# Optimization experiments

Measured on AMD Instinct MI355X. Metric: run time of the kernel, lower is better.

Reference implementation:

```python
import jax, jax.numpy as jnp
import numpy as np

B, S, H = 2, 2048, 1024
NUM_HEAD = 16
HEAD = H // NUM_HEAD
NEG = -10000000000.0


def setup_inputs() -> dict:
    key = jax.random.key(0)
    ks = jax.random.split(key, 10)
    scale = 1.0 / np.sqrt(H)
    return {
        "query": jax.random.normal(ks[0], (B, S, H), jnp.float32),
        "key": jax.random.normal(ks[1], (B, S, H), jnp.float32),
        "value": jax.random.normal(ks[2], (B, S, H), jnp.float32),
        "mask": jax.random.randint(ks[3], (B, S), 0, 2, jnp.int32),
        "Wq": jax.random.normal(ks[4], (H, H), jnp.float32) * scale,
        "bq": jnp.zeros((H,), jnp.float32),
        "Wk": jax.random.normal(ks[5], (H, H), jnp.float32) * scale,
        "bk": jnp.zeros((H,), jnp.float32),
        "Wv": jax.random.normal(ks[6], (H, H), jnp.float32) * scale,
        "bv": jnp.zeros((H,), jnp.float32),
    }


def reference(query, key, value, mask, Wq, bq, Wk, bk, Wv, bv):
    b, s, h = query.shape
    # Linear projections (torch Linear: x @ W.T + b), split into heads -> [b, nh, s, hd]
    def proj(x, W, bias):
        y = x @ W.T + bias
        return y.reshape(b, s, NUM_HEAD, HEAD).transpose(0, 2, 1, 3)

    q = proj(query, Wq, bq)
    k = proj(key, Wk, bk)
    v = proj(value, Wv, bv)

    # NOTE: original module has NO 1/sqrt(head_dim) scaling -- faithful.
    attn_score = jnp.einsum("bhqd,bhkd->bhqk", q, k)  # [b, nh, s, s]
    # key-padding mask bias: 0 where mask==1, -1e10 where mask==0, broadcast over query dim
    bias_add = jnp.where(mask[:, None, None, :] == 0, NEG, 0.0).astype(attn_score.dtype)
    attn_score = attn_score + bias_add
    attn_ratio = jax.nn.softmax(attn_score, axis=-1)
    out = jnp.einsum("bhqk,bhkd->bhqd", attn_ratio, v)  # [b, nh, s, hd]
    out = out.transpose(0, 2, 1, 3).reshape(b, s, h)
    # Dropout is identity in eval mode; output_linear is defined but never used in forward.
    return out
```

## Files before the change

kernel.cpp:

```cpp
#include <hip/hip_runtime.h>

#define BATCH 2
#define S_LEN 2048
#define HDIM  1024
#define NHEAD 16
#define HD    64
#define NEGBIAS -1e10f

typedef __attribute__((ext_vector_type(8))) _Float16 half8;
typedef __attribute__((ext_vector_type(4))) float   f32x4;

__global__ __launch_bounds__(256) void proj_gemm_f16(
    const float* __restrict__ Xq, const float* __restrict__ Wq, const float* __restrict__ bq,
    const float* __restrict__ Xk, const float* __restrict__ Wk, const float* __restrict__ bk,
    const float* __restrict__ Xv, const float* __restrict__ Wv, const float* __restrict__ bv,
    _Float16* __restrict__ Qb, _Float16* __restrict__ Kb, _Float16* __restrict__ Vtb)
{
    const int z = blockIdx.z;
    const float* X    = (z == 0) ? Xq : (z == 1) ? Xk : Xv;
    const float* W    = (z == 0) ? Wq : (z == 1) ? Wk : Wv;
    const float* bias = (z == 0) ? bq : (z == 1) ? bk : bv;
    _Float16* Y       = (z == 0) ? Qb : (z == 1) ? Kb : Vtb;

    const int n0 = blockIdx.x * 128;
    const int m0 = blockIdx.y * 128;

    __shared__ __align__(16) _Float16 As[128][40];
    __shared__ __align__(16) _Float16 Bs[128][40];

    const int t    = threadIdx.x;
    const int w    = t >> 6;
    const int lane = t & 63;
    const int quad = lane >> 4;
    const int lc   = lane & 15;
    const int wm   = (w >> 1) * 64;
    const int wn   = (w & 1) * 64;

    const f32x4 fzero = {0.f, 0.f, 0.f, 0.f};
    f32x4 acc[4][4];
#pragma unroll
    for (int i = 0; i < 4; i++)
#pragma unroll
        for (int j = 0; j < 4; j++) acc[i][j] = fzero;

    const int srow = t >> 2;
    const int sc   = t & 3;

    for (int k0 = 0; k0 < HDIM; k0 += 32) {
#pragma unroll
        for (int half = 0; half < 2; half++) {
            int row = srow + half * 64;
            {
                const float* g = X + (size_t)(m0 + row) * HDIM + k0 + sc * 8;
                float4 a0 = *(const float4*)g;
                float4 a1 = *(const float4*)(g + 4);
                half8 v;
                v[0] = (_Float16)a0.x; v[1] = (_Float16)a0.y;
                v[2] = (_Float16)a0.z; v[3] = (_Float16)a0.w;
                v[4] = (_Float16)a1.x; v[5] = (_Float16)a1.y;
                v[6] = (_Float16)a1.z; v[7] = (_Float16)a1.w;
                *(half8*)&As[row][sc * 8] = v;
            }
            {
                const float* g = W + (size_t)(n0 + row) * HDIM + k0 + sc * 8;
                float4 a0 = *(const float4*)g;
                float4 a1 = *(const float4*)(g + 4);
                half8 v;
                v[0] = (_Float16)a0.x; v[1] = (_Float16)a0.y;
                v[2] = (_Float16)a0.z; v[3] = (_Float16)a0.w;
                v[4] = (_Float16)a1.x; v[5] = (_Float16)a1.y;
                v[6] = (_Float16)a1.z; v[7] = (_Float16)a1.w;
                *(half8*)&Bs[row][sc * 8] = v;
            }
        }
        __syncthreads();

        half8 af[4], bf[4];
#pragma unroll
        for (int mt = 0; mt < 4; mt++)
            af[mt] = *(const half8*)&As[wm + mt * 16 + lc][quad * 8];
#pragma unroll
        for (int nt = 0; nt < 4; nt++)
            bf[nt] = *(const half8*)&Bs[wn + nt * 16 + lc][quad * 8];
#pragma unroll
        for (int mt = 0; mt < 4; mt++)
#pragma unroll
            for (int nt = 0; nt < 4; nt++)
                acc[mt][nt] = __builtin_amdgcn_mfma_f32_16x16x32_f16(
                    af[mt], bf[nt], acc[mt][nt], 0, 0, 0);
        __syncthreads();
    }

#pragma unroll
    for (int nt = 0; nt < 4; nt++) {
        const int n = n0 + wn + nt * 16 + lc;
        const float bv_ = bias[n];
        const int h = n >> 6, d = n & 63;
#pragma unroll
        for (int mt = 0; mt < 4; mt++) {
#pragma unroll
            for (int r = 0; r < 4; r++) {
                const int m = m0 + wm + mt * 16 + quad * 4 + r;
                const int b = m >> 11, s = m & (S_LEN - 1);
                const int bh = b * NHEAD + h;
                _Float16 val = (_Float16)(acc[mt][nt][r] + bv_);
                if (z == 2)
                    Y[((size_t)bh * HD + d) * S_LEN + s] = val;
                else
                    Y[((size_t)bh * S_LEN + s) * HD + d] = val;
            }
        }
    }
}

__global__ __launch_bounds__(256) void flash_attn_mfma(
    const _Float16* __restrict__ Qb, const _Float16* __restrict__ Kb,
    const _Float16* __restrict__ Vtb, const int* __restrict__ mask,
    float* __restrict__ out)
{
    const int qt = blockIdx.x & 31;
    const int bh = blockIdx.x >> 5;
    const int b  = bh >> 4;
    const int h  = bh & (NHEAD - 1);

    __shared__ __align__(16) _Float16 Ks [64][72];
    __shared__ __align__(16) _Float16 Vts[64][72];
    __shared__ __align__(16) _Float16 Ps [4][16][72];

    const int t    = threadIdx.x;
    const int w    = t >> 6;
    const int lane = t & 63;
    const int quad = lane >> 4;
    const int lc   = lane & 15;

    const _Float16* Kbase = Kb  + (size_t)bh * S_LEN * HD;
    const _Float16* Vbase = Vtb + (size_t)bh * HD * S_LEN;

    const int qrow = qt * 64 + w * 16 + lc;
    half8 qf[2];
#pragma unroll
    for (int s = 0; s < 2; s++)
        qf[s] = *(const half8*)(Qb + ((size_t)bh * S_LEN + qrow) * HD + s * 32 + quad * 8);

    const f32x4 fzero = {0.f, 0.f, 0.f, 0.f};
    f32x4 o[4];
#pragma unroll
    for (int nt = 0; nt < 4; nt++) o[nt] = fzero;
    float mrun[4] = {-3.0e38f, -3.0e38f, -3.0e38f, -3.0e38f};
    float lrun[4] = {0.f, 0.f, 0.f, 0.f};

    for (int kt = 0; kt < S_LEN; kt += 64) {
#pragma unroll
        for (int i = 0; i < 2; i++) {
            int c  = t + 256 * i;
            int rr = c >> 3;
            int cc = (c & 7) * 8;
            *(half8*)&Ks[rr][cc] =
                *(const half8*)(Kbase + (size_t)(kt + rr) * HD + cc);
            *(half8*)&Vts[rr][cc] =
                *(const half8*)(Vbase + (size_t)rr * S_LEN + kt + cc);
        }
        __syncthreads();

        f32x4 scf[4];
#pragma unroll
        for (int tt = 0; tt < 4; tt++) scf[tt] = fzero;
#pragma unroll
        for (int s = 0; s < 2; s++) {
#pragma unroll
            for (int tt = 0; tt < 4; tt++) {
                half8 kf = *(const half8*)&Ks[tt * 16 + lc][s * 32 + quad * 8];
                scf[tt] = __builtin_amdgcn_mfma_f32_16x16x32_f16(qf[s], kf, scf[tt], 0, 0, 0);
            }
        }

        float mb[4];
#pragma unroll
        for (int tt = 0; tt < 4; tt++)
            mb[tt] = mask[b * S_LEN + kt + tt * 16 + lc] ? 0.f : NEGBIAS;
#pragma unroll
        for (int tt = 0; tt < 4; tt++)
#pragma unroll
            for (int r = 0; r < 4; r++) scf[tt][r] += mb[tt];

#pragma unroll
        for (int r = 0; r < 4; r++) {
            float mx = scf[0][r];
#pragma unroll
            for (int tt = 1; tt < 4; tt++) mx = fmaxf(mx, scf[tt][r]);
            mx = fmaxf(mx, __shfl_xor(mx, 1));
            mx = fmaxf(mx, __shfl_xor(mx, 2));
            mx = fmaxf(mx, __shfl_xor(mx, 4));
            mx = fmaxf(mx, __shfl_xor(mx, 8));
            float mn = fmaxf(mrun[r], mx);
            float al = __expf(mrun[r] - mn);
            float ls = 0.f;
#pragma unroll
            for (int tt = 0; tt < 4; tt++) {
                float p = __expf(scf[tt][r] - mn);
                scf[tt][r] = p;
                ls += p;
            }
            ls += __shfl_xor(ls, 1);
            ls += __shfl_xor(ls, 2);
            ls += __shfl_xor(ls, 4);
            ls += __shfl_xor(ls, 8);
            lrun[r] = lrun[r] * al + ls;
            mrun[r] = mn;
#pragma unroll
            for (int nt = 0; nt < 4; nt++) o[nt][r] *= al;
        }

#pragma unroll
        for (int tt = 0; tt < 4; tt++)
#pragma unroll
            for (int r = 0; r < 4; r++)
                Ps[w][quad * 4 + r][tt * 16 + lc] = (_Float16)scf[tt][r];

#pragma unroll
        for (int s = 0; s < 2; s++) {
            half8 pf = *(const half8*)&Ps[w][lc][s * 32 + quad * 8];
#pragma unroll
            for (int nt = 0; nt < 4; nt++) {
                half8 vf = *(const half8*)&Vts[nt * 16 + lc][s * 32 + quad * 8];
                o[nt] = __builtin_amdgcn_mfma_f32_16x16x32_f16(pf, vf, o[nt], 0, 0, 0);
            }
        }
        __syncthreads();
    }

#pragma unroll
    for (int r = 0; r < 4; r++) {
        const int s_ = qt * 64 + w * 16 + quad * 4 + r;
        const float inv = 1.f / lrun[r];
        const size_t rowb = ((size_t)b * S_LEN + s_) * HDIM + h * HD;
#pragma unroll
        for (int nt = 0; nt < 4; nt++)
            out[rowb + nt * 16 + lc] = o[nt][r] * inv;
    }
}

extern "C" void kernel_launch(void* const* d_in, const int* in_sizes, int n_in,
                              void* d_out, int out_size, void* d_ws, size_t ws_size,
                              hipStream_t stream) {
    const float* query = (const float*)d_in[0];
    const float* key   = (const float*)d_in[1];
    const float* value = (const float*)d_in[2];
    const int*   mask  = (const int*)  d_in[3];
    const float* Wq    = (const float*)d_in[4];
    const float* bq    = (const float*)d_in[5];
    const float* Wk    = (const float*)d_in[6];
    const float* bk    = (const float*)d_in[7];
    const float* Wv    = (const float*)d_in[8];
    const float* bv    = (const float*)d_in[9];
    float* out = (float*)d_out;

    const size_t nElem = (size_t)BATCH * S_LEN * HDIM;
    if (ws_size < 3 * nElem * sizeof(_Float16)) return;
    _Float16* Qb  = (_Float16*)d_ws;
    _Float16* Kb  = Qb + nElem;
    _Float16* Vtb = Kb + nElem;

    dim3 gproj(HDIM / 128, (BATCH * S_LEN) / 128, 3);
    proj_gemm_f16<<<gproj, 256, 0, stream>>>(query, Wq, bq, key, Wk, bk,
                                             value, Wv, bv, Qb, Kb, Vtb);

    flash_attn_mfma<<<BATCH * NHEAD * (S_LEN / 64), 256, 0, stream>>>(
        Qb, Kb, Vtb, mask, out);
}
```

Measured before the change: 289.1 us.

## Pre-convert weights to fp16 and transpose MFMA operands in attention softmax

Adds a small kernel that converts the three weight matrices to fp16 once per call, so the projection GEMM loads half8 weights directly instead of converting fp32 tiles in every block. The attention kernel swaps the MFMA operand order so each lane holds one query row's scores. Row max and row sum then take two cross-lane shuffles instead of four per row. The key-padding bias is staged in shared memory, and the output is written as float4. This costs an extra kernel launch and workspace for the fp16 weights.

Result: faster. 252.1 us (-12.8%).

```diff
diff --git a/kernel.cpp b/kernel.cpp
--- a/kernel.cpp
+++ b/kernel.cpp
@@ -10,16 +10,35 @@
 typedef __attribute__((ext_vector_type(8))) _Float16 half8;
 typedef __attribute__((ext_vector_type(4))) float   f32x4;
 
+__global__ __launch_bounds__(256) void cvt_w(
+    const float* __restrict__ Wq, const float* __restrict__ Wk,
+    const float* __restrict__ Wv, _Float16* __restrict__ Wf)
+{
+    const int z = blockIdx.y;
+    const float* src = (z == 0) ? Wq : (z == 1) ? Wk : Wv;
+    _Float16* dst = Wf + (size_t)z * (HDIM * HDIM);
+    size_t i = ((size_t)blockIdx.x * 256 + threadIdx.x) * 8;
+    float4 a0 = *(const float4*)(src + i);
+    float4 a1 = *(const float4*)(src + i + 4);
+    half8 v;
+    v[0] = (_Float16)a0.x; v[1] = (_Float16)a0.y;
+    v[2] = (_Float16)a0.z; v[3] = (_Float16)a0.w;
+    v[4] = (_Float16)a1.x; v[5] = (_Float16)a1.y;
+    v[6] = (_Float16)a1.z; v[7] = (_Float16)a1.w;
+    *(half8*)(dst + i) = v;
+}
+
 __global__ __launch_bounds__(256) void proj_gemm_f16(
-    const float* __restrict__ Xq, const float* __restrict__ Wq, const float* __restrict__ bq,
-    const float* __restrict__ Xk, const float* __restrict__ Wk, const float* __restrict__ bk,
-    const float* __restrict__ Xv, const float* __restrict__ Wv, const float* __restrict__ bv,
+    const float* __restrict__ Xq, const float* __restrict__ Xk,
+    const float* __restrict__ Xv, const _Float16* __restrict__ Wf,
+    const float* __restrict__ bq, const float* __restrict__ bk,
+    const float* __restrict__ bv,
     _Float16* __restrict__ Qb, _Float16* __restrict__ Kb, _Float16* __restrict__ Vtb)
 {
     const int z = blockIdx.z;
     const float* X    = (z == 0) ? Xq : (z == 1) ? Xk : Xv;
-    const float* W    = (z == 0) ? Wq : (z == 1) ? Wk : Wv;
     const float* bias = (z == 0) ? bq : (z == 1) ? bk : bv;
+    const _Float16* Wz = Wf + (size_t)z * (HDIM * HDIM);
     _Float16* Y       = (z == 0) ? Qb : (z == 1) ? Kb : Vtb;
 
     const int n0 = blockIdx.x * 128;
@@ -61,17 +80,8 @@
                 v[6] = (_Float16)a1.z; v[7] = (_Float16)a1.w;
                 *(half8*)&As[row][sc * 8] = v;
             }
-            {
-                const float* g = W + (size_t)(n0 + row) * HDIM + k0 + sc * 8;
-                float4 a0 = *(const float4*)g;
-                float4 a1 = *(const float4*)(g + 4);
-                half8 v;
-                v[0] = (_Float16)a0.x; v[1] = (_Float16)a0.y;
-                v[2] = (_Float16)a0.z; v[3] = (_Float16)a0.w;
-                v[4] = (_Float16)a1.x; v[5] = (_Float16)a1.y;
-                v[6] = (_Float16)a1.z; v[7] = (_Float16)a1.w;
-                *(half8*)&Bs[row][sc * 8] = v;
-            }
+            *(half8*)&Bs[row][sc * 8] =
+                *(const half8*)(Wz + (size_t)(n0 + row) * HDIM + k0 + sc * 8);
         }
         __syncthreads();
 
@@ -126,6 +136,7 @@
     __shared__ __align__(16) _Float16 Ks [64][72];
     __shared__ __align__(16) _Float16 Vts[64][72];
     __shared__ __align__(16) _Float16 Ps [4][16][72];
+    __shared__ float biasS[64];
 
     const int t    = threadIdx.x;
     const int w    = t >> 6;
@@ -146,8 +157,8 @@
     f32x4 o[4];
 #pragma unroll
     for (int nt = 0; nt < 4; nt++) o[nt] = fzero;
-    float mrun[4] = {-3.0e38f, -3.0e38f, -3.0e38f, -3.0e38f};
-    float lrun[4] = {0.f, 0.f, 0.f, 0.f};
+    float mrun = -3.0e38f;
+    float lrun = 0.f;
 
     for (int kt = 0; kt < S_LEN; kt += 64) {
 #pragma unroll
@@ -160,6 +171,7 @@
             *(half8*)&Vts[rr][cc] =
                 *(const half8*)(Vbase + (size_t)rr * S_LEN + kt + cc);
         }
+        if (t < 64) biasS[t] = mask[b * S_LEN + kt + t] ? 0.f : NEGBIAS;
         __syncthreads();
 
         f32x4 scf[4];
@@ -170,52 +182,50 @@
 #pragma unroll
             for (int tt = 0; tt < 4; tt++) {
                 half8 kf = *(const half8*)&Ks[tt * 16 + lc][s * 32 + quad * 8];
-                scf[tt] = __builtin_amdgcn_mfma_f32_16x16x32_f16(qf[s], kf, scf[tt], 0, 0, 0);
-            }
-        }
-
-        float mb[4];
+                scf[tt] = __builtin_amdgcn_mfma_f32_16x16x32_f16(kf, qf[s], scf[tt], 0, 0, 0);
+            }
+        }
+
+#pragma unroll
+        for (int tt = 0; tt < 4; tt++) {
+            float4 b4 = *(const float4*)&biasS[tt * 16 + quad * 4];
+            scf[tt][0] += b4.x; scf[tt][1] += b4.y;
+            scf[tt][2] += b4.z; scf[tt][3] += b4.w;
+        }
+
+        float mx = scf[0][0];
 #pragma unroll
         for (int tt = 0; tt < 4; tt++)
-            mb[tt] = mask[b * S_LEN + kt + tt * 16 + lc] ? 0.f : NEGBIAS;
+#pragma unroll
+            for (int r = 0; r < 4; r++) mx = fmaxf(mx, scf[tt][r]);
+        mx = fmaxf(mx, __shfl_xor(mx, 16));
+        mx = fmaxf(mx, __shfl_xor(mx, 32));
+
+        float mn = fmaxf(mrun, mx);
+        float al = __expf(mrun - mn);
+        float ls = 0.f;
 #pragma unroll
         for (int tt = 0; tt < 4; tt++)
 #pragma unroll
-            for (int r = 0; r < 4; r++) scf[tt][r] += mb[tt];
-
-#pragma unroll
-        for (int r = 0; r < 4; r++) {
-            float mx = scf[0][r];
-#pragma unroll
-            for (int tt = 1; tt < 4; tt++) mx = fmaxf(mx, scf[tt][r]);
-            mx = fmaxf(mx, __shfl_xor(mx, 1));
-            mx = fmaxf(mx, __shfl_xor(mx, 2));
-            mx = fmaxf(mx, __shfl_xor(mx, 4));
-            mx = fmaxf(mx, __shfl_xor(mx, 8));
-            float mn = fmaxf(mrun[r], mx);
-            float al = __expf(mrun[r] - mn);
-            float ls = 0.f;
-#pragma unroll
-            for (int tt = 0; tt < 4; tt++) {
+            for (int r = 0; r < 4; r++) {
                 float p = __expf(scf[tt][r] - mn);
                 scf[tt][r] = p;
                 ls += p;
             }
-            ls += __shfl_xor(ls, 1);
-            ls += __shfl_xor(ls, 2);
-            ls += __shfl_xor(ls, 4);
-            ls += __shfl_xor(ls, 8);
-            lrun[r] = lrun[r] * al + ls;
-            mrun[r] = mn;
-#pragma unroll
-            for (int nt = 0; nt < 4; nt++) o[nt][r] *= al;
+        ls += __shfl_xor(ls, 16);
+        ls += __shfl_xor(ls, 32);
+        lrun = lrun * al + ls;
+        mrun = mn;
+#pragma unroll
+        for (int nt = 0; nt < 4; nt++) {
+            o[nt][0] *= al; o[nt][1] *= al; o[nt][2] *= al; o[nt][3] *= al;
         }
 
 #pragma unroll
         for (int tt = 0; tt < 4; tt++)
 #pragma unroll
             for (int r = 0; r < 4; r++)
-                Ps[w][quad * 4 + r][tt * 16 + lc] = (_Float16)scf[tt][r];
+                Ps[w][lc][tt * 16 + quad * 4 + r] = (_Float16)scf[tt][r];
 
 #pragma unroll
         for (int s = 0; s < 2; s++) {
@@ -223,20 +233,20 @@
 #pragma unroll
             for (int nt = 0; nt < 4; nt++) {
                 half8 vf = *(const half8*)&Vts[nt * 16 + lc][s * 32 + quad * 8];
-                o[nt] = __builtin_amdgcn_mfma_f32_16x16x32_f16(pf, vf, o[nt], 0, 0, 0);
-            }
-        }
-        __syncthreads();
-    }
-
-#pragma unroll
-    for (int r = 0; r < 4; r++) {
-        const int s_ = qt * 64 + w * 16 + quad * 4 + r;
-        const float inv = 1.f / lrun[r];
-        const size_t rowb = ((size_t)b * S_LEN + s_) * HDIM + h * HD;
-#pragma unroll
-        for (int nt = 0; nt < 4; nt++)
-            out[rowb + nt * 16 + lc] = o[nt][r] * inv;
+                o[nt] = __builtin_amdgcn_mfma_f32_16x16x32_f16(vf, pf, o[nt], 0, 0, 0);
+            }
+        }
+        __syncthreads();
+    }
+
+    const float inv = 1.f / lrun;
+    const size_t rowb = ((size_t)b * S_LEN + qrow) * HDIM + h * HD;
+#pragma unroll
+    for (int nt = 0; nt < 4; nt++) {
+        float4 v;
+        v.x = o[nt][0] * inv; v.y = o[nt][1] * inv;
+        v.z = o[nt][2] * inv; v.w = o[nt][3] * inv;
+        *(float4*)&out[rowb + nt * 16 + quad * 4] = v;
     }
 }
 
@@ -256,14 +266,19 @@
     float* out = (float*)d_out;
 
     const size_t nElem = (size_t)BATCH * S_LEN * HDIM;
-    if (ws_size < 3 * nElem * sizeof(_Float16)) return;
+    const size_t wElem = (size_t)HDIM * HDIM;
+    if (ws_size < (3 * nElem + 3 * wElem) * sizeof(_Float16)) return;
     _Float16* Qb  = (_Float16*)d_ws;
     _Float16* Kb  = Qb + nElem;
     _Float16* Vtb = Kb + nElem;
+    _Float16* Wf  = Vtb + nElem;
+
+    dim3 gcvt(wElem / (256 * 8), 3);
+    cvt_w<<<gcvt, 256, 0, stream>>>(Wq, Wk, Wv, Wf);
 
     dim3 gproj(HDIM / 128, (BATCH * S_LEN) / 128, 3);
-    proj_gemm_f16<<<gproj, 256, 0, stream>>>(query, Wq, bq, key, Wk, bk,
-                                             value, Wv, bv, Qb, Kb, Vtb);
+    proj_gemm_f16<<<gproj, 256, 0, stream>>>(query, key, value, Wf,
+                                             bq, bk, bv, Qb, Kb, Vtb);
 
     flash_attn_mfma<<<BATCH * NHEAD * (S_LEN / 64), 256, 0, stream>>>(
         Qb, Kb, Vtb, mask, out);
```
